# Kernel tuning notes

Measured on AMD Instinct MI355X. Metric: run time of the kernel, lower is better.

Reference implementation:

```python
import jax, jax.numpy as jnp
import numpy as np

MAX_REL = 32
NPE = 16
NRBF = 16
KNN = 32

def _layer_norm(x, g, b, eps=1e-5):
    mu = jnp.mean(x, axis=-1, keepdims=True)
    var = jnp.mean((x - mu) ** 2, axis=-1, keepdims=True)
    return (x - mu) * jax.lax.rsqrt(var + eps) * g + b

def _forward(dist_ca, omega, theta, phi, dihedral, mask_angle, mask, S, residue_idx, chain_encoding_all, pos_W, pos_b, edge_W, ln_e_g, ln_e_b, embed_tab, node_W, node_b, ln_n_g, ln_n_b):
    B, L, _ = dist_ca.shape
    # kNN graph from masked CA distances (smallest-K, ascending -> matches torch.topk largest=False)
    D = mask_angle * dist_ca
    D_max = jnp.max(D, axis=-1, keepdims=True)
    D_adjust = D + (1.0 - mask_angle) * D_max
    neg_vals, E_idx = jax.lax.top_k(-D_adjust, KNN)
    D_neighbors = -neg_vals                                     # [B,L,K]
    # 7 pairwise scalar edge channels, gathered at neighbor indices
    offset = (residue_idx[:, :, None] - residue_idx[:, None, :]).astype(jnp.float32)
    feats = jnp.stack([offset, jnp.cos(omega), jnp.sin(omega), jnp.cos(theta), jnp.sin(theta), jnp.cos(phi), jnp.sin(phi)], axis=0)  # [7,B,L,L]
    gathered = jnp.take_along_axis(feats, E_idx[None], axis=3)  # [7,B,L,K]
    edge_s = jax.lax.stop_gradient(gathered).astype(jnp.int32)  # torch .long(): truncate toward zero
    same_chain = (chain_encoding_all[:, :, None] == chain_encoding_all[:, None, :]).astype(jnp.int32)
    E_chains = jnp.take_along_axis(same_chain, E_idx, axis=2)[None]  # [1,B,L,K], broadcasts like tile(7,1,1)
    d = jnp.clip(edge_s + MAX_REL, 0, 2 * MAX_REL) * E_chains + (1 - E_chains) * (2 * MAX_REL + 1)
    E_pos = pos_W[d] + pos_b                                    # one_hot(d,66) @ W == row gather; [7,B,L,K,NPE]
    # rearrange '(n b) l t c -> b l t (n c)'
    E_pos = jnp.transpose(E_pos, (1, 2, 3, 0, 4)).reshape(B, L, KNN, 7 * NPE)
    # RBF of neighbor distances
    mu = jnp.linspace(2.0, 22.0, NRBF)
    sigma = (22.0 - 2.0) / NRBF
    RBF = jnp.exp(-(((D_neighbors[..., None] - mu) / sigma) ** 2))  # [B,L,K,NRBF]
    E = jnp.concatenate([E_pos, RBF], axis=-1) @ edge_W          # [B,L,K,128]
    E = _layer_norm(E, ln_e_g, ln_e_b)
    # node features: embedding(22->6) cat dihedral(6) -> linear(12->128) -> LN
    V = jnp.concatenate([embed_tab[S], dihedral], axis=-1) @ node_W + node_b
    V = _layer_norm(V, ln_n_g, ln_n_b)
    return V, E, E_idx

def setup_inputs():
    key = jax.random.key(0)
    ks = jax.random.split(key, 12)
    B, L, EF = 4, 2048, 128
    inp = {}
    inp["dist_ca"] = jax.random.uniform(ks[0], (B, L, L), jnp.float32) * 20.0 + 2.0
    inp["omega"] = jax.random.normal(ks[1], (B, L, L), jnp.float32)
    inp["theta"] = jax.random.normal(ks[2], (B, L, L), jnp.float32)
    inp["phi"] = jax.random.normal(ks[3], (B, L, L), jnp.float32)
    inp["dihedral"] = jax.random.normal(ks[4], (B, L, 6), jnp.float32)
    inp["mask_angle"] = jnp.ones((B, L, L), jnp.float32)
    inp["mask"] = jnp.ones((B, L), jnp.float32)
    inp["S"] = jax.random.randint(ks[5], (B, L), 0, 22)
    inp["residue_idx"] = jnp.arange(B * L, dtype=jnp.int32).reshape(B, L)
    inp["chain_encoding_all"] = jax.random.randint(ks[6], (B, L), 0, 4)
    # learned parameters (torch Linear weight transposed to [in,out])
    inp["pos_W"] = jax.random.normal(ks[7], (2 * MAX_REL + 2, NPE), jnp.float32) * 0.05
    inp["pos_b"] = jnp.zeros((NPE,), jnp.float32)
    inp["edge_W"] = jax.random.normal(ks[8], (7 * NPE + NRBF, EF), jnp.float32) * 0.05
    inp["ln_e_g"] = jnp.ones((EF,), jnp.float32)
    inp["ln_e_b"] = jnp.zeros((EF,), jnp.float32)
    inp["embed_tab"] = (jax.random.normal(ks[9], (22, 6), jnp.float32) * 0.5).at[21].set(0.0)  # padding_idx=21
    inp["node_W"] = jax.random.normal(ks[10], (12, EF), jnp.float32) * 0.1
    inp["node_b"] = jnp.zeros((EF,), jnp.float32)
    inp["ln_n_g"] = jnp.ones((EF,), jnp.float32)
    inp["ln_n_b"] = jnp.zeros((EF,), jnp.float32)
    return inp

def reference(dist_ca, omega, theta, phi, dihedral, mask_angle, mask, S, residue_idx, chain_encoding_all, pos_W, pos_b, edge_W, ln_e_g, ln_e_b, embed_tab, node_W, node_b, ln_n_g, ln_n_b):
    return _forward(dist_ca, omega, theta, phi, dihedral, mask_angle, mask, S, residue_idx, chain_encoding_all, pos_W, pos_b, edge_W, ln_e_g, ln_e_b, embed_tab, node_W, node_b, ln_n_g, ln_n_b)
```

## Files before the change

kernel.cpp:

```cpp
#include <hip/hip_runtime.h>
#include <hip/hip_bf16.h>
#include <math.h>

namespace {
constexpr int Ln   = 2048;
constexpr int Kn   = 32;
constexpr int EFn  = 128;
constexpr int ROWS = 4 * Ln;
constexpr size_t V_ELEMS = (size_t)ROWS * EFn;
constexpr size_t E_ELEMS = (size_t)ROWS * Kn * EFn;
constexpr size_t IDX_OFF = V_ELEMS + E_ELEMS;

__device__ __forceinline__ unsigned int orderKey(float f) {
  unsigned int u = __float_as_uint(f);
  return (u & 0x80000000u) ? ~u : (u | 0x80000000u);
}
__device__ __forceinline__ float keyToFloat(unsigned int k) {
  unsigned int u = (k & 0x80000000u) ? (k & 0x7fffffffu) : ~k;
  return __uint_as_float(u);
}
__device__ __forceinline__ unsigned long long u64min(unsigned long long a, unsigned long long b) {
  return a < b ? a : b;
}
}

__global__ void pf_tab(const float* __restrict__ pos_W, const float* __restrict__ pos_b,
                       const float* __restrict__ edge_W, float* __restrict__ T) {
  int n = blockIdx.x / 66, dd = blockIdx.x % 66, c = threadIdx.x;
  float acc = 0.f;
#pragma unroll
  for (int m = 0; m < 16; m++)
    acc += (pos_W[dd * 16 + m] + pos_b[m]) * edge_W[(n * 16 + m) * EFn + c];
  T[(size_t)(n * 66 + dd) * EFn + c] = acc;
}

__global__ __launch_bounds__(256) void pf_main(
    const float* __restrict__ dist_ca, const float* __restrict__ omega,
    const float* __restrict__ theta, const float* __restrict__ phi,
    const float* __restrict__ dihedral, const float* __restrict__ mask_angle,
    const int* __restrict__ Sarr, const int* __restrict__ ridx,
    const int* __restrict__ chain, const float* __restrict__ T,
    const float* __restrict__ edge_W, const float* __restrict__ ln_e_g,
    const float* __restrict__ ln_e_b, const float* __restrict__ embed_tab,
    const float* __restrict__ node_W, const float* __restrict__ node_b,
    const float* __restrict__ ln_n_g, const float* __restrict__ ln_n_b,
    float* __restrict__ out) {
  __shared__ unsigned int s_keys[Ln];
  __shared__ unsigned int s_hist[256];
  __shared__ unsigned long long s_cand[64];
  __shared__ unsigned long long s_w64[4];
  __shared__ float s_mx[4], s_mn2[4], s_mx2[4];
  __shared__ float s_v4[4];
  __shared__ int s_nidx[Kn];
  __shared__ float s_nval[Kn];
  __shared__ int s_d7[Kn * 8];
  __shared__ int s_bsel, s_tot, s_cnt;

  const int tid = threadIdx.x;
  const int lane = tid & 63, wid = tid >> 6;
  const int r = blockIdx.x;
  const int b = r >> 11;
  const size_t rowoff = (size_t)r * Ln;

  float Dv[8], Mv[8];
  float lmax = -3.4e38f;
#pragma unroll
  for (int m = 0; m < 8; m++) {
    int j = tid + (m << 8);
    float mk = mask_angle[rowoff + j];
    float dd = mk * dist_ca[rowoff + j];
    Dv[m] = dd; Mv[m] = mk;
    lmax = fmaxf(lmax, dd);
  }
#pragma unroll
  for (int o = 32; o; o >>= 1) lmax = fmaxf(lmax, __shfl_xor(lmax, o));
  if (!lane) s_mx[wid] = lmax;
  __syncthreads();
  const float Dmax = fmaxf(fmaxf(s_mx[0], s_mx[1]), fmaxf(s_mx[2], s_mx[3]));

  float lmin = 3.4e38f; lmax = -3.4e38f;
#pragma unroll
  for (int m = 0; m < 8; m++) {
    float adj = Dv[m] + (1.0f - Mv[m]) * Dmax;
    Dv[m] = adj;
    s_keys[tid + (m << 8)] = orderKey(adj);
    lmin = fminf(lmin, adj); lmax = fmaxf(lmax, adj);
  }
#pragma unroll
  for (int o = 32; o; o >>= 1) {
    lmin = fminf(lmin, __shfl_xor(lmin, o));
    lmax = fmaxf(lmax, __shfl_xor(lmax, o));
  }
  if (!lane) { s_mn2[wid] = lmin; s_mx2[wid] = lmax; }
  s_hist[tid] = 0u;
  __syncthreads();
  const float m0 = fminf(fminf(s_mn2[0], s_mn2[1]), fminf(s_mn2[2], s_mn2[3]));
  const float M0 = fmaxf(fmaxf(s_mx2[0], s_mx2[1]), fmaxf(s_mx2[2], s_mx2[3]));
  const float rng = M0 - m0;
  const float scale = (rng > 0.f) ? 255.0f / rng : 0.f;

  int binv[8];
#pragma unroll
  for (int m = 0; m < 8; m++) {
    int bin = (int)((Dv[m] - m0) * scale);
    bin = bin < 0 ? 0 : (bin > 255 ? 255 : bin);
    binv[m] = bin;
    atomicAdd(&s_hist[bin], 1u);
  }
  __syncthreads();
  for (int off = 1; off < 256; off <<= 1) {
    unsigned int u = 0;
    if (tid >= off) u = s_hist[tid - off];
    __syncthreads();
    if (tid >= off) s_hist[tid] += u;
    __syncthreads();
  }
  {
    unsigned int cum = s_hist[tid];
    unsigned int cump = tid ? s_hist[tid - 1] : 0u;
    if (cum >= (unsigned)Kn && cump < (unsigned)Kn) { s_bsel = tid; s_tot = (int)cum; }
    if (!tid) s_cnt = 0;
  }
  __syncthreads();
  const int bsel = s_bsel;
  const int tot = s_tot;

  if (tot <= 64) {
#pragma unroll
    for (int m = 0; m < 8; m++) {
      if (binv[m] <= bsel) {
        int p = atomicAdd(&s_cnt, 1);
        s_cand[p] = ((unsigned long long)orderKey(Dv[m]) << 16) | (unsigned)(tid + (m << 8));
      }
    }
  }
  __syncthreads();

  if (tot <= 64) {
    if (tid < 64) {
      unsigned long long v = (tid < tot) ? s_cand[tid] : ~0ull;
#pragma unroll
      for (int size = 2; size <= 64; size <<= 1) {
        for (int stride = size >> 1; stride > 0; stride >>= 1) {
          unsigned long long p = __shfl_xor(v, stride);
          bool keepMin = (((tid & stride) == 0) == ((tid & size) == 0));
          v = ((v < p) != keepMin) ? p : v;
        }
      }
      if (tid < Kn) {
        s_nidx[tid] = (int)(v & 0xffffull);
        s_nval[tid] = keyToFloat((unsigned int)(v >> 16));
      }
    }
  } else {
    for (int t = 0; t < Kn; t++) {
      unsigned long long lm = ~0ull;
#pragma unroll
      for (int m = 0; m < 8; m++) {
        int j = tid + (m << 8);
        unsigned long long kk = ((unsigned long long)s_keys[j] << 16) | (unsigned)j;
        lm = u64min(lm, kk);
      }
#pragma unroll
      for (int o = 32; o; o >>= 1) lm = u64min(lm, __shfl_xor(lm, o));
      if (!lane) s_w64[wid] = lm;
      __syncthreads();
      unsigned long long g = u64min(u64min(s_w64[0], s_w64[1]), u64min(s_w64[2], s_w64[3]));
      int j = (int)(g & 0xffffull);
      if (tid == (j & 255)) s_keys[j] = 0xffffffffu;
      if (!tid) { s_nidx[t] = j; s_nval[t] = keyToFloat((unsigned int)(g >> 16)); }
      __syncthreads();
    }
  }
  __syncthreads();

  if (tid < Kn)
    out[IDX_OFF + (size_t)r * Kn + tid] = (float)s_nidx[tid];

  const int ri_i = ridx[r];
  const int ch_i = chain[r];
  if (tid < Kn) {
    int j = s_nidx[tid];
    int rj = ridx[(size_t)b * Ln + j];
    int sc = (ch_i == chain[(size_t)b * Ln + j]) ? 1 : 0;
    int e0 = (int)((float)(ri_i - rj));
    int d0 = e0 + 32; d0 = d0 < 0 ? 0 : (d0 > 64 ? 64 : d0);
    s_d7[tid * 8 + 0] = sc ? d0 : 65;
    size_t pij = rowoff + j;
    float om = omega[pij], th = theta[pij], ph = phi[pij];
    float vals[6] = { cosf(om), sinf(om), cosf(th), sinf(th), cosf(ph), sinf(ph) };
#pragma unroll
    for (int n = 0; n < 6; n++) {
      int e = (int)vals[n];
      int d = e + 32; d = d < 0 ? 0 : (d > 64 ? 64 : d);
      s_d7[tid * 8 + 1 + n] = sc ? d : 65;
    }
  }
  __syncthreads();

  {
    const int k = tid >> 3, sub = tid & 7, c0 = sub << 4;
    float acc[16];
    {
      const float* Tp = T + (size_t)s_d7[k * 8 + 0] * EFn + c0;
#pragma unroll
      for (int m = 0; m < 16; m++) acc[m] = Tp[m];
    }
#pragma unroll
    for (int n = 1; n < 7; n++) {
      const float* Tp = T + (size_t)(n * 66 + s_d7[k * 8 + n]) * EFn + c0;
#pragma unroll
      for (int m = 0; m < 16; m++) acc[m] += Tp[m];
    }
    const float dv = s_nval[k];
#pragma unroll
    for (int rr = 0; rr < 16; rr++) {
      float mu = 2.0f + (20.0f / 15.0f) * (float)rr;
      float t = (dv - mu) * 0.8f;
      float rb = expf(-t * t);
      const float* W2 = edge_W + (size_t)(112 + rr) * EFn + c0;
#pragma unroll
      for (int m = 0; m < 16; m++) acc[m] = fmaf(rb, W2[m], acc[m]);
    }
    float s1 = 0.f, s2 = 0.f;
#pragma unroll
    for (int m = 0; m < 16; m++) { s1 += acc[m]; s2 += acc[m] * acc[m]; }
#pragma unroll
    for (int o = 1; o < 8; o <<= 1) { s1 += __shfl_xor(s1, o); s2 += __shfl_xor(s2, o); }
    const float mean = s1 * (1.0f / 128.0f);
    float var = s2 * (1.0f / 128.0f) - mean * mean;
    var = fmaxf(var, 0.f);
    const float inv = rsqrtf(var + 1e-5f);
    float y[16];
#pragma unroll
    for (int m = 0; m < 16; m++)
      y[m] = (acc[m] - mean) * inv * ln_e_g[c0 + m] + ln_e_b[c0 + m];
    float4* dst = (float4*)(out + V_ELEMS + ((size_t)(r * Kn + k) * EFn + c0));
    dst[0] = make_float4(y[0],  y[1],  y[2],  y[3]);
    dst[1] = make_float4(y[4],  y[5],  y[6],  y[7]);
    dst[2] = make_float4(y[8],  y[9],  y[10], y[11]);
    dst[3] = make_float4(y[12], y[13], y[14], y[15]);
  }

  float a = 0.f;
  if (tid < EFn) {
    const int c = tid;
    const int sv = Sarr[r];
    a = node_b[c];
#pragma unroll
    for (int m = 0; m < 6; m++) a = fmaf(embed_tab[sv * 6 + m], node_W[m * EFn + c], a);
#pragma unroll
    for (int m = 0; m < 6; m++) a = fmaf(dihedral[(size_t)r * 6 + m], node_W[(6 + m) * EFn + c], a);
    float s1 = a, s2 = a * a;
#pragma unroll
    for (int o = 32; o; o >>= 1) { s1 += __shfl_xor(s1, o); s2 += __shfl_xor(s2, o); }
    if (!lane) { s_v4[wid * 2] = s1; s_v4[wid * 2 + 1] = s2; }
  }
  __syncthreads();
  if (tid < EFn) {
    const float S1 = s_v4[0] + s_v4[2], S2 = s_v4[1] + s_v4[3];
    const float mean = S1 * (1.0f / 128.0f);
    float var = S2 * (1.0f / 128.0f) - mean * mean;
    var = fmaxf(var, 0.f);
    const float inv = rsqrtf(var + 1e-5f);
    const float yv = (a - mean) * inv * ln_n_g[tid] + ln_n_b[tid];
    out[(size_t)r * EFn + tid] = yv;
  }
}

extern "C" void kernel_launch(void* const* d_in, const int* in_sizes, int n_in,
                              void* d_out, int out_size, void* d_ws, size_t ws_size,
                              hipStream_t stream) {
  (void)in_sizes; (void)n_in; (void)out_size; (void)ws_size;
  const float* dist_ca    = (const float*)d_in[0];
  const float* omega      = (const float*)d_in[1];
  const float* theta      = (const float*)d_in[2];
  const float* phi        = (const float*)d_in[3];
  const float* dihedral   = (const float*)d_in[4];
  const float* mask_angle = (const float*)d_in[5];
  const int*   S          = (const int*)d_in[7];
  const int*   ridx       = (const int*)d_in[8];
  const int*   chain      = (const int*)d_in[9];
  const float* pos_W      = (const float*)d_in[10];
  const float* pos_b      = (const float*)d_in[11];
  const float* edge_W     = (const float*)d_in[12];
  const float* ln_e_g     = (const float*)d_in[13];
  const float* ln_e_b     = (const float*)d_in[14];
  const float* embed_tab  = (const float*)d_in[15];
  const float* node_W     = (const float*)d_in[16];
  const float* node_b     = (const float*)d_in[17];
  const float* ln_n_g     = (const float*)d_in[18];
  const float* ln_n_b     = (const float*)d_in[19];

  float* T = (float*)d_ws;

  pf_tab<<<7 * 66, 128, 0, stream>>>(pos_W, pos_b, edge_W, T);
  pf_main<<<ROWS, 256, 0, stream>>>(dist_ca, omega, theta, phi, dihedral, mask_angle,
                                    S, ridx, chain, T, edge_W, ln_e_g, ln_e_b,
                                    embed_tab, node_W, node_b, ln_n_g, ln_n_b,
                                    (float*)d_out);
}
```

Before: 509.6 us.

## Vectorize row loads, stage RBF weights in LDS, use warp-scan histogram

Each thread now reads dist_ca and mask_angle as contiguous float4 values with nontemporal loads, which changes the element-to-thread mapping. Because keys stay in registers, the shared-memory key array is dropped. The 256-bin prefix sum becomes a single-wavefront shuffle scan instead of a barrier loop. The RBF weight rows and LayerNorm parameters are staged in swizzled LDS, and the 6 angle features are split across 128 threads. Node-feature work is moved ahead of the edge computation, and edge outputs use nontemporal stores.

Result: faster. 486.5 us (-4.5%).

```diff
diff --git a/kernel.cpp b/kernel.cpp
--- a/kernel.cpp
+++ b/kernel.cpp
@@ -1,5 +1,4 @@
 #include <hip/hip_runtime.h>
-#include <hip/hip_bf16.h>
 #include <math.h>
 
 namespace {
@@ -11,6 +10,8 @@
 constexpr size_t E_ELEMS = (size_t)ROWS * Kn * EFn;
 constexpr size_t IDX_OFF = V_ELEMS + E_ELEMS;
 
+typedef float f32x4 __attribute__((ext_vector_type(4)));
+
 __device__ __forceinline__ unsigned int orderKey(float f) {
   unsigned int u = __float_as_uint(f);
   return (u & 0x80000000u) ? ~u : (u | 0x80000000u);
@@ -21,6 +22,9 @@
 }
 __device__ __forceinline__ unsigned long long u64min(unsigned long long a, unsigned long long b) {
   return a < b ? a : b;
+}
+__device__ __forceinline__ int swzChunk(int q) {
+  return (q & ~3) | ((q + (q >> 2)) & 3);
 }
 }
 
@@ -45,8 +49,9 @@
     const float* __restrict__ node_W, const float* __restrict__ node_b,
     const float* __restrict__ ln_n_g, const float* __restrict__ ln_n_b,
     float* __restrict__ out) {
-  __shared__ unsigned int s_keys[Ln];
-  __shared__ unsigned int s_hist[256];
+  __shared__ __align__(16) float s_W2[16 * EFn];
+  __shared__ __align__(16) float s_lng[EFn], s_lnb[EFn];
+  __shared__ __align__(16) unsigned int s_hist[256];
   __shared__ unsigned long long s_cand[64];
   __shared__ unsigned long long s_w64[4];
   __shared__ float s_mx[4], s_mn2[4], s_mx2[4];
@@ -62,16 +67,38 @@
   const int b = r >> 11;
   const size_t rowoff = (size_t)r * Ln;
 
+#pragma unroll
+  for (int it = 0; it < 2; it++) {
+    int idx = tid + (it << 8);
+    int rr = idx >> 5, q = idx & 31;
+    ((f32x4*)s_W2)[(rr << 5) + swzChunk(q)] =
+        ((const f32x4*)(edge_W + (size_t)(112 + rr) * EFn))[q];
+  }
+  if (tid < 64) {
+    int q = tid & 31;
+    const f32x4* src = (const f32x4*)((tid < 32) ? ln_e_g : ln_e_b);
+    f32x4* dst = (f32x4*)((tid < 32) ? s_lng : s_lnb);
+    dst[swzChunk(q)] = src[q];
+  }
+  s_hist[tid] = 0u;
+  if (!tid) s_cnt = 0;
+
   float Dv[8], Mv[8];
+  {
+    const f32x4* dp = (const f32x4*)(dist_ca + rowoff) + (tid << 1);
+    const f32x4* mp = (const f32x4*)(mask_angle + rowoff) + (tid << 1);
+    f32x4 d0 = __builtin_nontemporal_load(dp);
+    f32x4 d1 = __builtin_nontemporal_load(dp + 1);
+    f32x4 m0v = __builtin_nontemporal_load(mp);
+    f32x4 m1v = __builtin_nontemporal_load(mp + 1);
+#pragma unroll
+    for (int q = 0; q < 4; q++) { Mv[q] = m0v[q]; Mv[4 + q] = m1v[q]; }
+#pragma unroll
+    for (int q = 0; q < 4; q++) { Dv[q] = m0v[q] * d0[q]; Dv[4 + q] = m1v[q] * d1[q]; }
+  }
   float lmax = -3.4e38f;
 #pragma unroll
-  for (int m = 0; m < 8; m++) {
-    int j = tid + (m << 8);
-    float mk = mask_angle[rowoff + j];
-    float dd = mk * dist_ca[rowoff + j];
-    Dv[m] = dd; Mv[m] = mk;
-    lmax = fmaxf(lmax, dd);
-  }
+  for (int m = 0; m < 8; m++) lmax = fmaxf(lmax, Dv[m]);
 #pragma unroll
   for (int o = 32; o; o >>= 1) lmax = fmaxf(lmax, __shfl_xor(lmax, o));
   if (!lane) s_mx[wid] = lmax;
@@ -81,9 +108,8 @@
   float lmin = 3.4e38f; lmax = -3.4e38f;
 #pragma unroll
   for (int m = 0; m < 8; m++) {
-    float adj = Dv[m] + (1.0f - Mv[m]) * Dmax;
+    float adj = fmaf(1.0f - Mv[m], Dmax, Dv[m]);
     Dv[m] = adj;
-    s_keys[tid + (m << 8)] = orderKey(adj);
     lmin = fminf(lmin, adj); lmax = fmaxf(lmax, adj);
   }
 #pragma unroll
@@ -92,7 +118,6 @@
     lmax = fmaxf(lmax, __shfl_xor(lmax, o));
   }
   if (!lane) { s_mn2[wid] = lmin; s_mx2[wid] = lmax; }
-  s_hist[tid] = 0u;
   __syncthreads();
   const float m0 = fminf(fminf(s_mn2[0], s_mn2[1]), fminf(s_mn2[2], s_mn2[3]));
   const float M0 = fmaxf(fmaxf(s_mx2[0], s_mx2[1]), fmaxf(s_mx2[2], s_mx2[3]));
@@ -108,18 +133,24 @@
     atomicAdd(&s_hist[bin], 1u);
   }
   __syncthreads();
-  for (int off = 1; off < 256; off <<= 1) {
-    unsigned int u = 0;
-    if (tid >= off) u = s_hist[tid - off];
-    __syncthreads();
-    if (tid >= off) s_hist[tid] += u;
-    __syncthreads();
-  }
-  {
-    unsigned int cum = s_hist[tid];
-    unsigned int cump = tid ? s_hist[tid - 1] : 0u;
-    if (cum >= (unsigned)Kn && cump < (unsigned)Kn) { s_bsel = tid; s_tot = (int)cum; }
-    if (!tid) s_cnt = 0;
+
+  if (wid == 0) {
+    uint4 h = ((const uint4*)s_hist)[lane];
+    unsigned c1 = h.x + h.y, c2 = c1 + h.z, c3 = c2 + h.w;
+    unsigned pre = c3;
+#pragma unroll
+    for (int o = 1; o < 64; o <<= 1) {
+      unsigned u = __shfl_up(pre, o);
+      if (lane >= o) pre += u;
+    }
+    unsigned excl = pre - c3;
+    unsigned cums[4]  = {excl + h.x, excl + c1, excl + c2, excl + c3};
+    unsigned prevs[4] = {excl, excl + h.x, excl + c1, excl + c2};
+#pragma unroll
+    for (int q = 0; q < 4; q++)
+      if (cums[q] >= (unsigned)Kn && prevs[q] < (unsigned)Kn) {
+        s_bsel = (lane << 2) + q; s_tot = (int)cums[q];
+      }
   }
   __syncthreads();
   const int bsel = s_bsel;
@@ -130,7 +161,7 @@
     for (int m = 0; m < 8; m++) {
       if (binv[m] <= bsel) {
         int p = atomicAdd(&s_cnt, 1);
-        s_cand[p] = ((unsigned long long)orderKey(Dv[m]) << 16) | (unsigned)(tid + (m << 8));
+        s_cand[p] = ((unsigned long long)orderKey(Dv[m]) << 16) | (unsigned)((tid << 3) + m);
       }
     }
   }
@@ -157,8 +188,8 @@
       unsigned long long lm = ~0ull;
 #pragma unroll
       for (int m = 0; m < 8; m++) {
-        int j = tid + (m << 8);
-        unsigned long long kk = ((unsigned long long)s_keys[j] << 16) | (unsigned)j;
+        unsigned long long kk =
+            ((unsigned long long)orderKey(Dv[m]) << 16) | (unsigned)((tid << 3) + m);
         lm = u64min(lm, kk);
       }
 #pragma unroll
@@ -167,50 +198,79 @@
       __syncthreads();
       unsigned long long g = u64min(u64min(s_w64[0], s_w64[1]), u64min(s_w64[2], s_w64[3]));
       int j = (int)(g & 0xffffull);
-      if (tid == (j & 255)) s_keys[j] = 0xffffffffu;
+      {
+        bool own = ((j >> 3) == tid);
+        int jm = j & 7;
+#pragma unroll
+        for (int m = 0; m < 8; m++)
+          if (own && jm == m) Dv[m] = 3.4e38f;
+      }
       if (!tid) { s_nidx[t] = j; s_nval[t] = keyToFloat((unsigned int)(g >> 16)); }
       __syncthreads();
     }
   }
   __syncthreads();
 
+  const int ri_i = ridx[r];
+  const int ch_i = chain[r];
   if (tid < Kn)
     out[IDX_OFF + (size_t)r * Kn + tid] = (float)s_nidx[tid];
-
-  const int ri_i = ridx[r];
-  const int ch_i = chain[r];
-  if (tid < Kn) {
-    int j = s_nidx[tid];
-    int rj = ridx[(size_t)b * Ln + j];
-    int sc = (ch_i == chain[(size_t)b * Ln + j]) ? 1 : 0;
-    int e0 = (int)((float)(ri_i - rj));
-    int d0 = e0 + 32; d0 = d0 < 0 ? 0 : (d0 > 64 ? 64 : d0);
-    s_d7[tid * 8 + 0] = sc ? d0 : 65;
-    size_t pij = rowoff + j;
-    float om = omega[pij], th = theta[pij], ph = phi[pij];
-    float vals[6] = { cosf(om), sinf(om), cosf(th), sinf(th), cosf(ph), sinf(ph) };
-#pragma unroll
-    for (int n = 0; n < 6; n++) {
-      int e = (int)vals[n];
-      int d = e + 32; d = d < 0 ? 0 : (d > 64 ? 64 : d);
-      s_d7[tid * 8 + 1 + n] = sc ? d : 65;
-    }
-  }
-  __syncthreads();
+  if (tid < 128) {
+    const int k = tid & 31;
+    const int grp = tid >> 5;
+    const int j = s_nidx[k];
+    const int sc = (ch_i == chain[(size_t)b * Ln + j]) ? 1 : 0;
+    if (grp == 0) {
+      int rj = ridx[(size_t)b * Ln + j];
+      int d0 = ri_i - rj + 32;
+      d0 = d0 < 0 ? 0 : (d0 > 64 ? 64 : d0);
+      s_d7[(k << 3) + 0] = sc ? d0 : 65;
+    } else {
+      const float* src = (grp == 1) ? omega : (grp == 2) ? theta : phi;
+      float v = src[rowoff + j];
+      float cva = cosf(v), sva = sinf(v);
+      int dc = (int)cva + 32; dc = dc < 0 ? 0 : (dc > 64 ? 64 : dc);
+      int ds_ = (int)sva + 32; ds_ = ds_ < 0 ? 0 : (ds_ > 64 ? 64 : ds_);
+      s_d7[(k << 3) + (grp << 1) - 1] = sc ? dc : 65;
+      s_d7[(k << 3) + (grp << 1)]     = sc ? ds_ : 65;
+    }
+  }
+  __syncthreads();
+
+  float a = 0.f;
+  if (tid < EFn) {
+    const int c = tid;
+    const int sv2 = Sarr[r];
+    a = node_b[c];
+#pragma unroll
+    for (int m = 0; m < 6; m++) a = fmaf(embed_tab[sv2 * 6 + m], node_W[m * EFn + c], a);
+#pragma unroll
+    for (int m = 0; m < 6; m++) a = fmaf(dihedral[(size_t)r * 6 + m], node_W[(6 + m) * EFn + c], a);
+    float s1 = a, s2 = a * a;
+#pragma unroll
+    for (int o = 32; o; o >>= 1) { s1 += __shfl_xor(s1, o); s2 += __shfl_xor(s2, o); }
+    if (!lane) { s_v4[wid * 2] = s1; s_v4[wid * 2 + 1] = s2; }
+  }
 
   {
     const int k = tid >> 3, sub = tid & 7, c0 = sub << 4;
     float acc[16];
     {
-      const float* Tp = T + (size_t)s_d7[k * 8 + 0] * EFn + c0;
-#pragma unroll
-      for (int m = 0; m < 16; m++) acc[m] = Tp[m];
+      const f32x4* Tp = (const f32x4*)(T + (size_t)s_d7[k << 3] * EFn + c0);
+      f32x4 a0 = Tp[0], a1 = Tp[1], a2 = Tp[2], a3 = Tp[3];
+#pragma unroll
+      for (int q = 0; q < 4; q++) {
+        acc[q] = a0[q]; acc[4 + q] = a1[q]; acc[8 + q] = a2[q]; acc[12 + q] = a3[q];
+      }
     }
 #pragma unroll
     for (int n = 1; n < 7; n++) {
-      const float* Tp = T + (size_t)(n * 66 + s_d7[k * 8 + n]) * EFn + c0;
-#pragma unroll
-      for (int m = 0; m < 16; m++) acc[m] += Tp[m];
+      const f32x4* Tp = (const f32x4*)(T + (size_t)(n * 66 + s_d7[(k << 3) + n]) * EFn + c0);
+      f32x4 a0 = Tp[0], a1 = Tp[1], a2 = Tp[2], a3 = Tp[3];
+#pragma unroll
+      for (int q = 0; q < 4; q++) {
+        acc[q] += a0[q]; acc[4 + q] += a1[q]; acc[8 + q] += a2[q]; acc[12 + q] += a3[q];
+      }
     }
     const float dv = s_nval[k];
 #pragma unroll
@@ -218,9 +278,14 @@
       float mu = 2.0f + (20.0f / 15.0f) * (float)rr;
       float t = (dv - mu) * 0.8f;
       float rb = expf(-t * t);
-      const float* W2 = edge_W + (size_t)(112 + rr) * EFn + c0;
-#pragma unroll
-      for (int m = 0; m < 16; m++) acc[m] = fmaf(rb, W2[m], acc[m]);
+      const f32x4* Wr = (const f32x4*)(s_W2 + (rr << 7));
+#pragma unroll
+      for (int w = 0; w < 4; w++) {
+        f32x4 wv = Wr[(sub << 2) | ((w + sub) & 3)];
+#pragma unroll
+        for (int q = 0; q < 4; q++)
+          acc[(w << 2) + q] = fmaf(rb, wv[q], acc[(w << 2) + q]);
+      }
     }
     float s1 = 0.f, s2 = 0.f;
 #pragma unroll
@@ -231,40 +296,28 @@
     float var = s2 * (1.0f / 128.0f) - mean * mean;
     var = fmaxf(var, 0.f);
     const float inv = rsqrtf(var + 1e-5f);
-    float y[16];
-#pragma unroll
-    for (int m = 0; m < 16; m++)
-      y[m] = (acc[m] - mean) * inv * ln_e_g[c0 + m] + ln_e_b[c0 + m];
-    float4* dst = (float4*)(out + V_ELEMS + ((size_t)(r * Kn + k) * EFn + c0));
-    dst[0] = make_float4(y[0],  y[1],  y[2],  y[3]);
-    dst[1] = make_float4(y[4],  y[5],  y[6],  y[7]);
-    dst[2] = make_float4(y[8],  y[9],  y[10], y[11]);
-    dst[3] = make_float4(y[12], y[13], y[14], y[15]);
-  }
-
-  float a = 0.f;
-  if (tid < EFn) {
-    const int c = tid;
-    const int sv = Sarr[r];
-    a = node_b[c];
-#pragma unroll
-    for (int m = 0; m < 6; m++) a = fmaf(embed_tab[sv * 6 + m], node_W[m * EFn + c], a);
-#pragma unroll
-    for (int m = 0; m < 6; m++) a = fmaf(dihedral[(size_t)r * 6 + m], node_W[(6 + m) * EFn + c], a);
-    float s1 = a, s2 = a * a;
-#pragma unroll
-    for (int o = 32; o; o >>= 1) { s1 += __shfl_xor(s1, o); s2 += __shfl_xor(s2, o); }
-    if (!lane) { s_v4[wid * 2] = s1; s_v4[wid * 2 + 1] = s2; }
-  }
-  __syncthreads();
+    f32x4* dst = (f32x4*)(out + V_ELEMS + ((size_t)(r * Kn + k) * EFn + c0));
+#pragma unroll
+    for (int w = 0; w < 4; w++) {
+      int p = (sub << 2) | ((w + sub) & 3);
+      f32x4 g = ((const f32x4*)s_lng)[p];
+      f32x4 bb = ((const f32x4*)s_lnb)[p];
+      f32x4 o4;
+#pragma unroll
+      for (int q = 0; q < 4; q++)
+        o4[q] = (acc[(w << 2) + q] - mean) * inv * g[q] + bb[q];
+      __builtin_nontemporal_store(o4, dst + w);
+    }
+  }
+  __syncthreads();
+
   if (tid < EFn) {
     const float S1 = s_v4[0] + s_v4[2], S2 = s_v4[1] + s_v4[3];
     const float mean = S1 * (1.0f / 128.0f);
     float var = S2 * (1.0f / 128.0f) - mean * mean;
     var = fmaxf(var, 0.f);
     const float inv = rsqrtf(var + 1e-5f);
-    const float yv = (a - mean) * inv * ln_n_g[tid] + ln_n_b[tid];
-    out[(size_t)r * EFn + tid] = yv;
+    out[(size_t)r * EFn + tid] = (a - mean) * inv * ln_n_g[tid] + ln_n_b[tid];
   }
 }
 
```
